# Kernel optimization log

Measured on AMD Instinct MI355X. Metric: run time of the kernel, lower is better.

The kernel has to match this reference:

```python
import jax, jax.numpy as jnp
import numpy as np

HEADS = 16

def split_heads(v, heads):
    # NOTE: faithful to the source: reshape [B,S,D] -> [B,S,h_dim,heads], then
    # transpose to [B,heads,S,h_dim]. This interleaves channels across heads
    # (different from the standard [B,S,heads,h_dim] split).
    B, S, D = v.shape
    hd = D // heads
    return v.reshape(B, S, hd, heads).transpose(0, 3, 1, 2)

def merge_heads(v):
    # [B,heads,S,h_dim] -> transpose [B,S,h_dim,heads] -> reshape [B,S,D]
    B, H, S, hd = v.shape
    return v.transpose(0, 2, 3, 1).reshape(B, S, H * hd)

def setup_inputs() -> dict:
    key = jax.random.key(0)
    ks = jax.random.split(key, 5)
    B, S, D = 2, 2048, 1024
    return {
        "x": jax.random.normal(ks[0], (B, S, D), dtype=jnp.float32),
        "qw": jax.random.normal(ks[1], (D, D), dtype=jnp.float32),
        "kw": jax.random.normal(ks[2], (D, D), dtype=jnp.float32),
        "vw": jax.random.normal(ks[3], (D, D), dtype=jnp.float32),
        "ow": jax.random.normal(ks[4], (D, D), dtype=jnp.float32),
    }

def reference(x, qw, kw, vw, ow):
    B, S, D = x.shape
    Q = split_heads(x @ qw, HEADS)  # [B,H,S,hd]
    K = split_heads(x @ kw, HEADS)
    V = split_heads(x @ vw, HEADS)
    # NOTE: scale is 1/sqrt(dim), NOT 1/sqrt(head_dim), as in the source.
    scale = 1.0 / jnp.sqrt(jnp.float32(D))
    score = jnp.einsum("bhqd,bhkd->bhqk", Q, K) * scale  # [B,H,S,S]
    causal = jnp.tril(jnp.ones((1, 1, S, S), dtype=score.dtype))
    score = score - 1e10 * (1.0 - causal)
    weights = jax.nn.softmax(score, axis=-1)
    attn = jnp.einsum("bhqk,bhkd->bhqd", weights, V)
    return merge_heads(attn) @ ow
```

## Files before the change

kernel.cpp:

```cpp
#include <hip/hip_runtime.h>


typedef __bf16 bf16x8 __attribute__((ext_vector_type(8)));
typedef float  f32x4  __attribute__((ext_vector_type(4)));

#define S_LEN  2048
#define DMODEL 1024
#define NHEADS 16
#define HDIM   64
#define LOG2E  1.44269504088896340736f

__device__ __forceinline__ void gll16(const __bf16* g, __bf16* l) {
    __builtin_amdgcn_global_load_lds(
        (const __attribute__((address_space(1))) unsigned int*)g,
        (__attribute__((address_space(3))) unsigned int*)l, 16, 0, 0);
}

__global__ __launch_bounds__(256) void conv_split(const float* __restrict__ x,
                                                  __bf16* __restrict__ hi,
                                                  __bf16* __restrict__ lo, int n4) {
    int i = blockIdx.x * 256 + threadIdx.x;
    if (i >= n4) return;
    float4 v = ((const float4*)x)[i];
    __bf16 h0 = (__bf16)v.x, h1 = (__bf16)v.y, h2 = (__bf16)v.z, h3 = (__bf16)v.w;
    bf16x8 dummy;
    (void)dummy;
    ushort4 hh, ll;
    hh.x = __builtin_bit_cast(unsigned short, h0);
    hh.y = __builtin_bit_cast(unsigned short, h1);
    hh.z = __builtin_bit_cast(unsigned short, h2);
    hh.w = __builtin_bit_cast(unsigned short, h3);
    ll.x = __builtin_bit_cast(unsigned short, (__bf16)(v.x - (float)h0));
    ll.y = __builtin_bit_cast(unsigned short, (__bf16)(v.y - (float)h1));
    ll.z = __builtin_bit_cast(unsigned short, (__bf16)(v.z - (float)h2));
    ll.w = __builtin_bit_cast(unsigned short, (__bf16)(v.w - (float)h3));
    ((ushort4*)hi)[i] = hh;
    ((ushort4*)lo)[i] = ll;
}

__global__ __launch_bounds__(256) void transpose_all(
    const float* __restrict__ qw, const float* __restrict__ kw,
    const float* __restrict__ vw, const float* __restrict__ ow,
    __bf16* __restrict__ qwthi, __bf16* __restrict__ qwtlo,
    __bf16* __restrict__ kwthi, __bf16* __restrict__ kwtlo,
    __bf16* __restrict__ vwt,  __bf16* __restrict__ owt) {
    __shared__ float tile[32][33];
    int z = blockIdx.z;
    const float* w = (z == 0) ? qw : (z == 1) ? kw : (z == 2) ? vw : ow;
    int n0 = blockIdx.x * 32, k0 = blockIdx.y * 32;
    int tx = threadIdx.x & 31, ty = threadIdx.x >> 5;
#pragma unroll
    for (int i = 0; i < 32; i += 8)
        tile[ty + i][tx] = w[(k0 + ty + i) * DMODEL + n0 + tx];
    __syncthreads();
#pragma unroll
    for (int i = 0; i < 32; i += 8) {
        float f = tile[tx][ty + i];
        int k = k0 + tx, n = n0 + ty + i;
        if (z <= 1) {
            __bf16 fh = (__bf16)f;
            __bf16 fl = (__bf16)(f - (float)fh);
            int c = (n & 15) * 64 + (n >> 4);
            if (z == 0) { qwthi[c * DMODEL + k] = fh; qwtlo[c * DMODEL + k] = fl; }
            else        { kwthi[c * DMODEL + k] = fh; kwtlo[c * DMODEL + k] = fl; }
        } else if (z == 2) {
            vwt[n * DMODEL + k] = (__bf16)f;
        } else {
            int ck = (k & 15) * 64 + (k >> 4);
            owt[n * DMODEL + ck] = (__bf16)f;
        }
    }
}

__global__ __launch_bounds__(256) void qkv_gemm(
    const __bf16* __restrict__ xhi, const __bf16* __restrict__ xlo,
    const __bf16* __restrict__ qwthi, const __bf16* __restrict__ qwtlo,
    const __bf16* __restrict__ kwthi, const __bf16* __restrict__ kwtlo,
    const __bf16* __restrict__ vwt,
    __bf16* __restrict__ Qhi, __bf16* __restrict__ Qlo,
    __bf16* __restrict__ Khi, __bf16* __restrict__ Klo,
    __bf16* __restrict__ Vt) {
    __shared__ __bf16 Ash[128][32], Asl[128][32], Bsh[128][32], Bsl[128][32];
    int mode = blockIdx.z;
    int tid  = threadIdx.x;
    int wave = tid >> 6, lane = tid & 63;
    int quad = lane >> 4, l15 = lane & 15;
    int wm = (wave >> 1) * 64, wn = (wave & 1) * 64;
    int grow = lane >> 2, gcol = (lane & 3) * 8;
    const int K = DMODEL;

    if (mode < 2) {
        const __bf16* Bh = mode ? kwthi : qwthi;
        const __bf16* Bl = mode ? kwtlo : qwtlo;
        int m0 = blockIdx.y * 128, n0 = blockIdx.x * 128;
        f32x4 acc[4][4] = {};
        for (int k0 = 0; k0 < K; k0 += 32) {
            __syncthreads();
#pragma unroll
            for (int ps = 0; ps < 2; ps++) {
                int row = ps * 64 + wave * 16;
                gll16(&xhi[(m0 + row + grow) * K + k0 + gcol], &Ash[row][0]);
                gll16(&xlo[(m0 + row + grow) * K + k0 + gcol], &Asl[row][0]);
                gll16(&Bh [(n0 + row + grow) * K + k0 + gcol], &Bsh[row][0]);
                gll16(&Bl [(n0 + row + grow) * K + k0 + gcol], &Bsl[row][0]);
            }
            __syncthreads();
            bf16x8 ah[4], al[4], bh[4], bl[4];
#pragma unroll
            for (int mi = 0; mi < 4; mi++) {
                ah[mi] = *(const bf16x8*)&Ash[wm + mi * 16 + l15][quad * 8];
                al[mi] = *(const bf16x8*)&Asl[wm + mi * 16 + l15][quad * 8];
            }
#pragma unroll
            for (int ni = 0; ni < 4; ni++) {
                bh[ni] = *(const bf16x8*)&Bsh[wn + ni * 16 + l15][quad * 8];
                bl[ni] = *(const bf16x8*)&Bsl[wn + ni * 16 + l15][quad * 8];
            }
#pragma unroll
            for (int mi = 0; mi < 4; mi++)
#pragma unroll
                for (int ni = 0; ni < 4; ni++) {
                    acc[mi][ni] = __builtin_amdgcn_mfma_f32_16x16x32_bf16(ah[mi], bh[ni], acc[mi][ni], 0, 0, 0);
                    acc[mi][ni] = __builtin_amdgcn_mfma_f32_16x16x32_bf16(ah[mi], bl[ni], acc[mi][ni], 0, 0, 0);
                    acc[mi][ni] = __builtin_amdgcn_mfma_f32_16x16x32_bf16(al[mi], bh[ni], acc[mi][ni], 0, 0, 0);
                }
        }
        float oscale = mode ? 1.0f : 0.03125f * LOG2E;
        __bf16* Ohi = mode ? Khi : Qhi;
        __bf16* Olo = mode ? Klo : Qlo;
#pragma unroll
        for (int mi = 0; mi < 4; mi++)
#pragma unroll
            for (int ni = 0; ni < 4; ni++)
#pragma unroll
                for (int rg = 0; rg < 4; rg++) {
                    int m = m0 + wm + mi * 16 + quad * 4 + rg;
                    int n = n0 + wn + ni * 16 + l15;
                    float v = acc[mi][ni][rg] * oscale;
                    size_t idx = (size_t)m * DMODEL + n;
                    __bf16 vh = (__bf16)v;
                    Ohi[idx] = vh;
                    Olo[idx] = (__bf16)(v - (float)vh);
                }
    } else {
        int ch0 = blockIdx.x * 128, xm0 = blockIdx.y * 128;
        f32x4 acc[4][4] = {};
        for (int k0 = 0; k0 < K; k0 += 32) {
            __syncthreads();
#pragma unroll
            for (int ps = 0; ps < 2; ps++) {
                int row = ps * 64 + wave * 16;
                gll16(&vwt[(ch0 + row + grow) * K + k0 + gcol], &Ash[row][0]);
                gll16(&xhi[(xm0 + row + grow) * K + k0 + gcol], &Bsh[row][0]);
            }
            __syncthreads();
            bf16x8 af[4], bfr[4];
#pragma unroll
            for (int mi = 0; mi < 4; mi++)
                af[mi] = *(const bf16x8*)&Ash[wm + mi * 16 + l15][quad * 8];
#pragma unroll
            for (int ni = 0; ni < 4; ni++)
                bfr[ni] = *(const bf16x8*)&Bsh[wn + ni * 16 + l15][quad * 8];
#pragma unroll
            for (int mi = 0; mi < 4; mi++)
#pragma unroll
                for (int ni = 0; ni < 4; ni++)
                    acc[mi][ni] = __builtin_amdgcn_mfma_f32_16x16x32_bf16(
                        af[mi], bfr[ni], acc[mi][ni], 0, 0, 0);
        }
#pragma unroll
        for (int mi = 0; mi < 4; mi++)
#pragma unroll
            for (int ni = 0; ni < 4; ni++)
#pragma unroll
                for (int rg = 0; rg < 4; rg++) {
                    int ch = ch0 + wm + mi * 16 + quad * 4 + rg;
                    int xm = xm0 + wn + ni * 16 + l15;
                    int b = xm >> 11, s = xm & 2047;
                    int h = ch & 15,  d = ch >> 4;
                    Vt[((size_t)(b * NHEADS + h) * HDIM + d) * S_LEN + s] =
                        (__bf16)acc[mi][ni][rg];
                }
    }
}

__global__ __launch_bounds__(256) void out_gemm(const __bf16* __restrict__ A,
                                                const __bf16* __restrict__ Bt,
                                                float* __restrict__ out) {
    __shared__ __bf16 As[64][32];
    __shared__ __bf16 Bs[128][32];
    int tid  = threadIdx.x;
    int wave = tid >> 6, lane = tid & 63;
    int quad = lane >> 4, l15 = lane & 15;
    int m0 = blockIdx.y * 64, n0 = blockIdx.x * 128;
    int wm = (wave >> 1) * 32, wn = (wave & 1) * 64;
    int grow = lane >> 2, gcol = (lane & 3) * 8;
    const int K = DMODEL;
    f32x4 acc[2][4] = {};

    for (int k0 = 0; k0 < K; k0 += 32) {
        __syncthreads();
        gll16(&A[(m0 + wave * 16 + grow) * K + k0 + gcol], &As[wave * 16][0]);
#pragma unroll
        for (int ps = 0; ps < 2; ps++) {
            int row = ps * 64 + wave * 16;
            gll16(&Bt[(n0 + row + grow) * K + k0 + gcol], &Bs[row][0]);
        }
        __syncthreads();
        bf16x8 af[2], bfr[4];
#pragma unroll
        for (int mi = 0; mi < 2; mi++)
            af[mi] = *(const bf16x8*)&As[wm + mi * 16 + l15][quad * 8];
#pragma unroll
        for (int ni = 0; ni < 4; ni++)
            bfr[ni] = *(const bf16x8*)&Bs[wn + ni * 16 + l15][quad * 8];
#pragma unroll
        for (int mi = 0; mi < 2; mi++)
#pragma unroll
            for (int ni = 0; ni < 4; ni++)
                acc[mi][ni] = __builtin_amdgcn_mfma_f32_16x16x32_bf16(
                    af[mi], bfr[ni], acc[mi][ni], 0, 0, 0);
    }

#pragma unroll
    for (int mi = 0; mi < 2; mi++)
#pragma unroll
        for (int ni = 0; ni < 4; ni++)
#pragma unroll
            for (int rg = 0; rg < 4; rg++) {
                int m = m0 + wm + mi * 16 + quad * 4 + rg;
                int n = n0 + wn + ni * 16 + l15;
                out[(size_t)m * DMODEL + n] = acc[mi][ni][rg];
            }
}

__global__ __launch_bounds__(256, 4) void flash_attn(const __bf16* __restrict__ Qhi,
                                                     const __bf16* __restrict__ Qlo,
                                                     const __bf16* __restrict__ Khi,
                                                     const __bf16* __restrict__ Klo,
                                                     const __bf16* __restrict__ Vt,
                                                     __bf16* __restrict__ attn) {
    int id  = blockIdx.x;
    int xcd = id & 7, r = id >> 3;
    int bh  = xcd + 8 * (r & 3);
    int t   = 31 - (r >> 2);
    int b = bh >> 4, h = bh & 15;
    const __bf16* Qh_hi = Qhi + (size_t)b * S_LEN * DMODEL + h * HDIM;
    const __bf16* Qh_lo = Qlo + (size_t)b * S_LEN * DMODEL + h * HDIM;
    const __bf16* Kh_hi = Khi + (size_t)b * S_LEN * DMODEL + h * HDIM;
    const __bf16* Kh_lo = Klo + (size_t)b * S_LEN * DMODEL + h * HDIM;
    const __bf16* Vh    = Vt  + (size_t)bh * HDIM * S_LEN;

    int tid = threadIdx.x, wave = tid >> 6, lane = tid & 63;
    int quad = lane >> 4, l15 = lane & 15;
    int iters = t + 1;

    __shared__ __bf16 KhF[8 * 64 * 8];
    __shared__ __bf16 KlF[8 * 64 * 8];
    __shared__ __bf16 VF [8 * 64 * 8];
    __shared__ __bf16 Ps[4][16][72];

    int c1  = tid >> 6, key = tid & 63;
    int inner = (c1 * 16 + (key & 15)) * 8;
    int rK    = (key >> 4);
    int kdst0 = rK * 512 + inner, kdst1 = (4 + rK) * 512 + inner;
    const __bf16* vrow = Vh + (size_t)key * S_LEN;

    int q0w = t * 64 + wave * 16;
    bf16x8 aqh0 = *(const bf16x8*)&Qh_hi[(size_t)(q0w + l15) * DMODEL + quad * 8];
    bf16x8 aqh1 = *(const bf16x8*)&Qh_hi[(size_t)(q0w + l15) * DMODEL + 32 + quad * 8];
    bf16x8 aql0 = *(const bf16x8*)&Qh_lo[(size_t)(q0w + l15) * DMODEL + quad * 8];
    bf16x8 aql1 = *(const bf16x8*)&Qh_lo[(size_t)(q0w + l15) * DMODEL + 32 + quad * 8];

    bf16x8 ones;
#pragma unroll
    for (int j = 0; j < 8; j++) ones[j] = (__bf16)1.0f;

    uint4 pk0, pk1, pl0, pl1, pv0, pv1;
    {
        const __bf16* sk = Kh_hi + (size_t)key * DMODEL;
        const __bf16* sl = Kh_lo + (size_t)key * DMODEL;
        pk0 = *(const uint4*)(sk + c1 * 8); pk1 = *(const uint4*)(sk + c1 * 8 + 32);
        pl0 = *(const uint4*)(sl + c1 * 8); pl1 = *(const uint4*)(sl + c1 * 8 + 32);
        pv0 = *(const uint4*)(vrow + c1 * 8); pv1 = *(const uint4*)(vrow + c1 * 8 + 32);
    }

    float m[4] = {-3e38f, -3e38f, -3e38f, -3e38f};
    f32x4 o[4] = {};
    f32x4 ol = {};
    int qrb = q0w + quad * 4;

    for (int i = 0; i < iters; i++) {
        int key0 = i * 64;
        bool diag = (i == iters - 1);

        __syncthreads();
        *(uint4*)&KhF[kdst0] = pk0;  *(uint4*)&KhF[kdst1] = pk1;
        *(uint4*)&KlF[kdst0] = pl0;  *(uint4*)&KlF[kdst1] = pl1;
        *(uint4*)&VF [kdst0] = pv0;  *(uint4*)&VF [kdst1] = pv1;
        __syncthreads();

        if (i + 1 < iters) {
            int key0n = (i + 1) * 64;
            const __bf16* sk = Kh_hi + (size_t)(key0n + key) * DMODEL;
            const __bf16* sl = Kh_lo + (size_t)(key0n + key) * DMODEL;
            pk0 = *(const uint4*)(sk + c1 * 8); pk1 = *(const uint4*)(sk + c1 * 8 + 32);
            pl0 = *(const uint4*)(sl + c1 * 8); pl1 = *(const uint4*)(sl + c1 * 8 + 32);
            pv0 = *(const uint4*)(vrow + key0n + c1 * 8);
            pv1 = *(const uint4*)(vrow + key0n + c1 * 8 + 32);
        }

        f32x4 sc[4] = {};
#pragma unroll
        for (int ni = 0; ni < 4; ni++) {
            bf16x8 kh0 = *(const bf16x8*)&KhF[(ni * 64 + lane) * 8];
            bf16x8 kh1 = *(const bf16x8*)&KhF[((4 + ni) * 64 + lane) * 8];
            bf16x8 kl0 = *(const bf16x8*)&KlF[(ni * 64 + lane) * 8];
            bf16x8 kl1 = *(const bf16x8*)&KlF[((4 + ni) * 64 + lane) * 8];
            sc[ni] = __builtin_amdgcn_mfma_f32_16x16x32_bf16(aqh0, kh0, sc[ni], 0, 0, 0);
            sc[ni] = __builtin_amdgcn_mfma_f32_16x16x32_bf16(aqh1, kh1, sc[ni], 0, 0, 0);
            sc[ni] = __builtin_amdgcn_mfma_f32_16x16x32_bf16(aqh0, kl0, sc[ni], 0, 0, 0);
            sc[ni] = __builtin_amdgcn_mfma_f32_16x16x32_bf16(aqh1, kl1, sc[ni], 0, 0, 0);
            sc[ni] = __builtin_amdgcn_mfma_f32_16x16x32_bf16(aql0, kh0, sc[ni], 0, 0, 0);
            sc[ni] = __builtin_amdgcn_mfma_f32_16x16x32_bf16(aql1, kh1, sc[ni], 0, 0, 0);
        }

        if (diag) {
#pragma unroll
            for (int ni = 0; ni < 4; ni++) {
                int keyi = key0 + ni * 16 + l15;
#pragma unroll
                for (int rg = 0; rg < 4; rg++)
                    if (keyi > qrb + rg) sc[ni][rg] = -1e30f;
            }
        }

#pragma unroll
        for (int rg = 0; rg < 4; rg++) {
            float mx = fmaxf(fmaxf(sc[0][rg], sc[1][rg]),
                             fmaxf(sc[2][rg], sc[3][rg]));
#pragma unroll
            for (int mm = 1; mm < 16; mm <<= 1)
                mx = fmaxf(mx, __shfl_xor(mx, mm, 64));
            float mnew  = fmaxf(m[rg], mx);
            float alpha = __builtin_amdgcn_exp2f(m[rg] - mnew);
            m[rg] = mnew;
#pragma unroll
            for (int ni = 0; ni < 4; ni++) {
                float px = __builtin_amdgcn_exp2f(sc[ni][rg] - mnew);
                Ps[wave][quad * 4 + rg][ni * 16 + l15] = (__bf16)px;
            }
            ol[rg] *= alpha;
#pragma unroll
            for (int ni = 0; ni < 4; ni++)
                o[ni][rg] *= alpha;
        }

#pragma unroll
        for (int step = 0; step < 2; step++) {
            bf16x8 ap = *(const bf16x8*)&Ps[wave][l15][step * 32 + quad * 8];
            ol = __builtin_amdgcn_mfma_f32_16x16x32_bf16(ap, ones, ol, 0, 0, 0);
#pragma unroll
            for (int ni = 0; ni < 4; ni++) {
                bf16x8 bv = *(const bf16x8*)&VF[((step * 4 + ni) * 64 + lane) * 8];
                o[ni] = __builtin_amdgcn_mfma_f32_16x16x32_bf16(ap, bv, o[ni], 0, 0, 0);
            }
        }
    }

#pragma unroll
    for (int rg = 0; rg < 4; rg++) {
        float inv = 1.0f / ol[rg];
        int q = q0w + quad * 4 + rg;
#pragma unroll
        for (int ni = 0; ni < 4; ni++) {
            attn[((size_t)b * S_LEN + q) * DMODEL + h * HDIM + ni * 16 + l15] =
                (__bf16)(o[ni][rg] * inv);
        }
    }
}

extern "C" void kernel_launch(void* const* d_in, const int* in_sizes, int n_in,
                              void* d_out, int out_size, void* d_ws, size_t ws_size,
                              hipStream_t stream) {
    const float* x  = (const float*)d_in[0];
    const float* qw = (const float*)d_in[1];
    const float* kw = (const float*)d_in[2];
    const float* vw = (const float*)d_in[3];
    const float* ow = (const float*)d_in[4];

    char* ws = (char*)d_ws;
    const size_t MB = 1024 * 1024;
    __bf16* xhi   = (__bf16*)(ws);
    __bf16* xlo   = (__bf16*)(ws + 8 * MB);
    __bf16* qwthi = (__bf16*)(ws + 16 * MB);
    __bf16* qwtlo = (__bf16*)(ws + 18 * MB);
    __bf16* kwthi = (__bf16*)(ws + 20 * MB);
    __bf16* kwtlo = (__bf16*)(ws + 22 * MB);
    __bf16* vwt   = (__bf16*)(ws + 24 * MB);
    __bf16* owt   = (__bf16*)(ws + 26 * MB);
    __bf16* Qhi_b = (__bf16*)(ws + 28 * MB);
    __bf16* Qlo_b = (__bf16*)(ws + 36 * MB);
    __bf16* Khi_b = (__bf16*)(ws + 44 * MB);
    __bf16* Klo_b = (__bf16*)(ws + 52 * MB);
    __bf16* Vtb   = (__bf16*)(ws + 60 * MB);
    __bf16* attnb = xlo;

    conv_split<<<4096, 256, 0, stream>>>(x, xhi, xlo, 4096 * 1024 / 4);
    transpose_all<<<dim3(32, 32, 4), 256, 0, stream>>>(
        qw, kw, vw, ow, qwthi, qwtlo, kwthi, kwtlo, vwt, owt);

    qkv_gemm<<<dim3(8, 32, 3), 256, 0, stream>>>(
        xhi, xlo, qwthi, qwtlo, kwthi, kwtlo, vwt,
        Qhi_b, Qlo_b, Khi_b, Klo_b, Vtb);

    flash_attn<<<1024, 256, 0, stream>>>(Qhi_b, Qlo_b, Khi_b, Klo_b, Vtb, attnb);

    out_gemm<<<dim3(8, 64), 256, 0, stream>>>(attnb, owt, (float*)d_out);
}
```

Baseline: 258.0 us.

## Double flash-attention query tile to 128 rows per block for K/V reuse

```diff
diff --git a/kernel.cpp b/kernel.cpp
--- a/kernel.cpp
+++ b/kernel.cpp
@@ -23,8 +23,6 @@
     if (i >= n4) return;
     float4 v = ((const float4*)x)[i];
     __bf16 h0 = (__bf16)v.x, h1 = (__bf16)v.y, h2 = (__bf16)v.z, h3 = (__bf16)v.w;
-    bf16x8 dummy;
-    (void)dummy;
     ushort4 hh, ll;
     hh.x = __builtin_bit_cast(unsigned short, h0);
     hh.y = __builtin_bit_cast(unsigned short, h1);
@@ -234,7 +232,7 @@
             }
 }
 
-__global__ __launch_bounds__(256, 4) void flash_attn(const __bf16* __restrict__ Qhi,
+__global__ __launch_bounds__(256, 3) void flash_attn(const __bf16* __restrict__ Qhi,
                                                      const __bf16* __restrict__ Qlo,
                                                      const __bf16* __restrict__ Khi,
                                                      const __bf16* __restrict__ Klo,
@@ -243,7 +241,7 @@
     int id  = blockIdx.x;
     int xcd = id & 7, r = id >> 3;
     int bh  = xcd + 8 * (r & 3);
-    int t   = 31 - (r >> 2);
+    int t   = 15 - (r >> 2);
     int b = bh >> 4, h = bh & 15;
     const __bf16* Qh_hi = Qhi + (size_t)b * S_LEN * DMODEL + h * HDIM;
     const __bf16* Qh_lo = Qlo + (size_t)b * S_LEN * DMODEL + h * HDIM;
@@ -253,12 +251,12 @@
 
     int tid = threadIdx.x, wave = tid >> 6, lane = tid & 63;
     int quad = lane >> 4, l15 = lane & 15;
-    int iters = t + 1;
+    int iters = 2 * t + 2;
 
     __shared__ __bf16 KhF[8 * 64 * 8];
     __shared__ __bf16 KlF[8 * 64 * 8];
     __shared__ __bf16 VF [8 * 64 * 8];
-    __shared__ __bf16 Ps[4][16][72];
+    __shared__ __bf16 Ps[4][32][72];
 
     int c1  = tid >> 6, key = tid & 63;
     int inner = (c1 * 16 + (key & 15)) * 8;
@@ -266,11 +264,16 @@
     int kdst0 = rK * 512 + inner, kdst1 = (4 + rK) * 512 + inner;
     const __bf16* vrow = Vh + (size_t)key * S_LEN;
 
-    int q0w = t * 64 + wave * 16;
-    bf16x8 aqh0 = *(const bf16x8*)&Qh_hi[(size_t)(q0w + l15) * DMODEL + quad * 8];
-    bf16x8 aqh1 = *(const bf16x8*)&Qh_hi[(size_t)(q0w + l15) * DMODEL + 32 + quad * 8];
-    bf16x8 aql0 = *(const bf16x8*)&Qh_lo[(size_t)(q0w + l15) * DMODEL + quad * 8];
-    bf16x8 aql1 = *(const bf16x8*)&Qh_lo[(size_t)(q0w + l15) * DMODEL + 32 + quad * 8];
+    int q0w = t * 128 + wave * 32;
+    bf16x8 aqh0[2], aqh1[2], aql0[2], aql1[2];
+#pragma unroll
+    for (int mi = 0; mi < 2; mi++) {
+        size_t qr = (size_t)(q0w + mi * 16 + l15) * DMODEL;
+        aqh0[mi] = *(const bf16x8*)&Qh_hi[qr + quad * 8];
+        aqh1[mi] = *(const bf16x8*)&Qh_hi[qr + 32 + quad * 8];
+        aql0[mi] = *(const bf16x8*)&Qh_lo[qr + quad * 8];
+        aql1[mi] = *(const bf16x8*)&Qh_lo[qr + 32 + quad * 8];
+    }
 
     bf16x8 ones;
 #pragma unroll
@@ -285,14 +288,13 @@
         pv0 = *(const uint4*)(vrow + c1 * 8); pv1 = *(const uint4*)(vrow + c1 * 8 + 32);
     }
 
-    float m[4] = {-3e38f, -3e38f, -3e38f, -3e38f};
-    f32x4 o[4] = {};
-    f32x4 ol = {};
-    int qrb = q0w + quad * 4;
+    float m[2][4] = {{-3e38f, -3e38f, -3e38f, -3e38f},
+                     {-3e38f, -3e38f, -3e38f, -3e38f}};
+    f32x4 o[2][4] = {};
+    f32x4 ol[2] = {};
 
     for (int i = 0; i < iters; i++) {
         int key0 = i * 64;
-        bool diag = (i == iters - 1);
 
         __syncthreads();
         *(uint4*)&KhF[kdst0] = pk0;  *(uint4*)&KhF[kdst1] = pk1;
@@ -310,74 +312,85 @@
             pv1 = *(const uint4*)(vrow + key0n + c1 * 8 + 32);
         }
 
-        f32x4 sc[4] = {};
+        f32x4 sc[2][4] = {};
 #pragma unroll
         for (int ni = 0; ni < 4; ni++) {
             bf16x8 kh0 = *(const bf16x8*)&KhF[(ni * 64 + lane) * 8];
             bf16x8 kh1 = *(const bf16x8*)&KhF[((4 + ni) * 64 + lane) * 8];
             bf16x8 kl0 = *(const bf16x8*)&KlF[(ni * 64 + lane) * 8];
             bf16x8 kl1 = *(const bf16x8*)&KlF[((4 + ni) * 64 + lane) * 8];
-            sc[ni] = __builtin_amdgcn_mfma_f32_16x16x32_bf16(aqh0, kh0, sc[ni], 0, 0, 0);
-            sc[ni] = __builtin_amdgcn_mfma_f32_16x16x32_bf16(aqh1, kh1, sc[ni], 0, 0, 0);
-            sc[ni] = __builtin_amdgcn_mfma_f32_16x16x32_bf16(aqh0, kl0, sc[ni], 0, 0, 0);
-            sc[ni] = __builtin_amdgcn_mfma_f32_16x16x32_bf16(aqh1, kl1, sc[ni], 0, 0, 0);
-            sc[ni] = __builtin_amdgcn_mfma_f32_16x16x32_bf16(aql0, kh0, sc[ni], 0, 0, 0);
-            sc[ni] = __builtin_amdgcn_mfma_f32_16x16x32_bf16(aql1, kh1, sc[ni], 0, 0, 0);
-        }
-
-        if (diag) {
-#pragma unroll
-            for (int ni = 0; ni < 4; ni++) {
-                int keyi = key0 + ni * 16 + l15;
-#pragma unroll
-                for (int rg = 0; rg < 4; rg++)
-                    if (keyi > qrb + rg) sc[ni][rg] = -1e30f;
-            }
-        }
-
-#pragma unroll
-        for (int rg = 0; rg < 4; rg++) {
-            float mx = fmaxf(fmaxf(sc[0][rg], sc[1][rg]),
-                             fmaxf(sc[2][rg], sc[3][rg]));
-#pragma unroll
-            for (int mm = 1; mm < 16; mm <<= 1)
-                mx = fmaxf(mx, __shfl_xor(mx, mm, 64));
-            float mnew  = fmaxf(m[rg], mx);
-            float alpha = __builtin_amdgcn_exp2f(m[rg] - mnew);
-            m[rg] = mnew;
-#pragma unroll
-            for (int ni = 0; ni < 4; ni++) {
-                float px = __builtin_amdgcn_exp2f(sc[ni][rg] - mnew);
-                Ps[wave][quad * 4 + rg][ni * 16 + l15] = (__bf16)px;
-            }
-            ol[rg] *= alpha;
-#pragma unroll
-            for (int ni = 0; ni < 4; ni++)
-                o[ni][rg] *= alpha;
+#pragma unroll
+            for (int mi = 0; mi < 2; mi++) {
+                sc[mi][ni] = __builtin_amdgcn_mfma_f32_16x16x32_bf16(aqh0[mi], kh0, sc[mi][ni], 0, 0, 0);
+                sc[mi][ni] = __builtin_amdgcn_mfma_f32_16x16x32_bf16(aqh1[mi], kh1, sc[mi][ni], 0, 0, 0);
+                sc[mi][ni] = __builtin_amdgcn_mfma_f32_16x16x32_bf16(aqh0[mi], kl0, sc[mi][ni], 0, 0, 0);
+                sc[mi][ni] = __builtin_amdgcn_mfma_f32_16x16x32_bf16(aqh1[mi], kl1, sc[mi][ni], 0, 0, 0);
+                sc[mi][ni] = __builtin_amdgcn_mfma_f32_16x16x32_bf16(aql0[mi], kh0, sc[mi][ni], 0, 0, 0);
+                sc[mi][ni] = __builtin_amdgcn_mfma_f32_16x16x32_bf16(aql1[mi], kh1, sc[mi][ni], 0, 0, 0);
+            }
+        }
+
+#pragma unroll
+        for (int mi = 0; mi < 2; mi++) {
+            int qrb = q0w + mi * 16 + quad * 4;
+            if (key0 + 63 > qrb) {
+#pragma unroll
+                for (int ni = 0; ni < 4; ni++) {
+                    int keyi = key0 + ni * 16 + l15;
+#pragma unroll
+                    for (int rg = 0; rg < 4; rg++)
+                        if (keyi > qrb + rg) sc[mi][ni][rg] = -1e30f;
+                }
+            }
+#pragma unroll
+            for (int rg = 0; rg < 4; rg++) {
+                float mx = fmaxf(fmaxf(sc[mi][0][rg], sc[mi][1][rg]),
+                                 fmaxf(sc[mi][2][rg], sc[mi][3][rg]));
+#pragma unroll
+                for (int mm = 1; mm < 16; mm <<= 1)
+                    mx = fmaxf(mx, __shfl_xor(mx, mm, 64));
+                float mnew  = fmaxf(m[mi][rg], mx);
+                float alpha = __builtin_amdgcn_exp2f(m[mi][rg] - mnew);
+                m[mi][rg] = mnew;
+#pragma unroll
+                for (int ni = 0; ni < 4; ni++) {
+                    float px = __builtin_amdgcn_exp2f(sc[mi][ni][rg] - mnew);
+                    Ps[wave][mi * 16 + quad * 4 + rg][ni * 16 + l15] = (__bf16)px;
+                }
+                ol[mi][rg] *= alpha;
+#pragma unroll
+                for (int ni = 0; ni < 4; ni++)
+                    o[mi][ni][rg] *= alpha;
+            }
         }
 
 #pragma unroll
         for (int step = 0; step < 2; step++) {
-            bf16x8 ap = *(const bf16x8*)&Ps[wave][l15][step * 32 + quad * 8];
-            ol = __builtin_amdgcn_mfma_f32_16x16x32_bf16(ap, ones, ol, 0, 0, 0);
+            bf16x8 ap0 = *(const bf16x8*)&Ps[wave][l15][step * 32 + quad * 8];
+            bf16x8 ap1 = *(const bf16x8*)&Ps[wave][16 + l15][step * 32 + quad * 8];
+            ol[0] = __builtin_amdgcn_mfma_f32_16x16x32_bf16(ap0, ones, ol[0], 0, 0, 0);
+            ol[1] = __builtin_amdgcn_mfma_f32_16x16x32_bf16(ap1, ones, ol[1], 0, 0, 0);
 #pragma unroll
             for (int ni = 0; ni < 4; ni++) {
                 bf16x8 bv = *(const bf16x8*)&VF[((step * 4 + ni) * 64 + lane) * 8];
-                o[ni] = __builtin_amdgcn_mfma_f32_16x16x32_bf16(ap, bv, o[ni], 0, 0, 0);
-            }
-        }
-    }
-
-#pragma unroll
-    for (int rg = 0; rg < 4; rg++) {
-        float inv = 1.0f / ol[rg];
-        int q = q0w + quad * 4 + rg;
-#pragma unroll
-        for (int ni = 0; ni < 4; ni++) {
-            attn[((size_t)b * S_LEN + q) * DMODEL + h * HDIM + ni * 16 + l15] =
-                (__bf16)(o[ni][rg] * inv);
-        }
-    }
+                o[0][ni] = __builtin_amdgcn_mfma_f32_16x16x32_bf16(ap0, bv, o[0][ni], 0, 0, 0);
+                o[1][ni] = __builtin_amdgcn_mfma_f32_16x16x32_bf16(ap1, bv, o[1][ni], 0, 0, 0);
+            }
+        }
+    }
+
+#pragma unroll
+    for (int mi = 0; mi < 2; mi++)
+#pragma unroll
+        for (int rg = 0; rg < 4; rg++) {
+            float inv = 1.0f / ol[mi][rg];
+            int q = q0w + mi * 16 + quad * 4 + rg;
+#pragma unroll
+            for (int ni = 0; ni < 4; ni++) {
+                attn[((size_t)b * S_LEN + q) * DMODEL + h * HDIM + ni * 16 + l15] =
+                    (__bf16)(o[mi][ni][rg] * inv);
+            }
+        }
 }
 
 extern "C" void kernel_launch(void* const* d_in, const int* in_sizes, int n_in,
@@ -414,7 +427,7 @@
         xhi, xlo, qwthi, qwtlo, kwthi, kwtlo, vwt,
         Qhi_b, Qlo_b, Khi_b, Klo_b, Vtb);
 
-    flash_attn<<<1024, 256, 0, stream>>>(Qhi_b, Qlo_b, Khi_b, Klo_b, Vtb, attnb);
+    flash_attn<<<512, 256, 0, stream>>>(Qhi_b, Qlo_b, Khi_b, Klo_b, Vtb, attnb);
 
     out_gemm<<<dim3(8, 64), 256, 0, stream>>>(attnb, owt, (float*)d_out);
 }
```

After: 325.8 us. 26.3% more time.

## Merge prep kernels into one launch and fuse Q/K projections sharing x tiles

Applied to the files above, without the earlier changes.

```diff
diff --git a/kernel.cpp b/kernel.cpp
--- a/kernel.cpp
+++ b/kernel.cpp
@@ -16,38 +16,38 @@
         (__attribute__((address_space(3))) unsigned int*)l, 16, 0, 0);
 }
 
-__global__ __launch_bounds__(256) void conv_split(const float* __restrict__ x,
-                                                  __bf16* __restrict__ hi,
-                                                  __bf16* __restrict__ lo, int n4) {
-    int i = blockIdx.x * 256 + threadIdx.x;
-    if (i >= n4) return;
-    float4 v = ((const float4*)x)[i];
-    __bf16 h0 = (__bf16)v.x, h1 = (__bf16)v.y, h2 = (__bf16)v.z, h3 = (__bf16)v.w;
-    bf16x8 dummy;
-    (void)dummy;
-    ushort4 hh, ll;
-    hh.x = __builtin_bit_cast(unsigned short, h0);
-    hh.y = __builtin_bit_cast(unsigned short, h1);
-    hh.z = __builtin_bit_cast(unsigned short, h2);
-    hh.w = __builtin_bit_cast(unsigned short, h3);
-    ll.x = __builtin_bit_cast(unsigned short, (__bf16)(v.x - (float)h0));
-    ll.y = __builtin_bit_cast(unsigned short, (__bf16)(v.y - (float)h1));
-    ll.z = __builtin_bit_cast(unsigned short, (__bf16)(v.z - (float)h2));
-    ll.w = __builtin_bit_cast(unsigned short, (__bf16)(v.w - (float)h3));
-    ((ushort4*)hi)[i] = hh;
-    ((ushort4*)lo)[i] = ll;
-}
-
-__global__ __launch_bounds__(256) void transpose_all(
+__global__ __launch_bounds__(256) void prep_all(
+    const float* __restrict__ x,
     const float* __restrict__ qw, const float* __restrict__ kw,
     const float* __restrict__ vw, const float* __restrict__ ow,
+    __bf16* __restrict__ xhi, __bf16* __restrict__ xlo,
     __bf16* __restrict__ qwthi, __bf16* __restrict__ qwtlo,
     __bf16* __restrict__ kwthi, __bf16* __restrict__ kwtlo,
     __bf16* __restrict__ vwt,  __bf16* __restrict__ owt) {
     __shared__ float tile[32][33];
-    int z = blockIdx.z;
+    int id = blockIdx.x;
+    if (id < 4096) {
+        int i = id * 256 + threadIdx.x;
+        float4 v = ((const float4*)x)[i];
+        __bf16 h0 = (__bf16)v.x, h1 = (__bf16)v.y, h2 = (__bf16)v.z, h3 = (__bf16)v.w;
+        ushort4 hh, ll;
+        hh.x = __builtin_bit_cast(unsigned short, h0);
+        hh.y = __builtin_bit_cast(unsigned short, h1);
+        hh.z = __builtin_bit_cast(unsigned short, h2);
+        hh.w = __builtin_bit_cast(unsigned short, h3);
+        ll.x = __builtin_bit_cast(unsigned short, (__bf16)(v.x - (float)h0));
+        ll.y = __builtin_bit_cast(unsigned short, (__bf16)(v.y - (float)h1));
+        ll.z = __builtin_bit_cast(unsigned short, (__bf16)(v.z - (float)h2));
+        ll.w = __builtin_bit_cast(unsigned short, (__bf16)(v.w - (float)h3));
+        ((ushort4*)xhi)[i] = hh;
+        ((ushort4*)xlo)[i] = ll;
+        return;
+    }
+    int rid = id - 4096;
+    int z = rid >> 10;
+    int bx = rid & 31, by = (rid >> 5) & 31;
     const float* w = (z == 0) ? qw : (z == 1) ? kw : (z == 2) ? vw : ow;
-    int n0 = blockIdx.x * 32, k0 = blockIdx.y * 32;
+    int n0 = bx * 32, k0 = by * 32;
     int tx = threadIdx.x & 31, ty = threadIdx.x >> 5;
 #pragma unroll
     for (int i = 0; i < 32; i += 8)
@@ -80,8 +80,8 @@
     __bf16* __restrict__ Qhi, __bf16* __restrict__ Qlo,
     __bf16* __restrict__ Khi, __bf16* __restrict__ Klo,
     __bf16* __restrict__ Vt) {
-    __shared__ __bf16 Ash[128][32], Asl[128][32], Bsh[128][32], Bsl[128][32];
-    int mode = blockIdx.z;
+    __shared__ __bf16 Ash[128][32], Asl[128][32];
+    __shared__ __bf16 Bqh[128][32], Bql[128][32], Bkh[128][32], Bkl[128][32];
     int tid  = threadIdx.x;
     int wave = tid >> 6, lane = tid & 63;
     int quad = lane >> 4, l15 = lane & 15;
@@ -89,23 +89,23 @@
     int grow = lane >> 2, gcol = (lane & 3) * 8;
     const int K = DMODEL;
 
-    if (mode < 2) {
-        const __bf16* Bh = mode ? kwthi : qwthi;
-        const __bf16* Bl = mode ? kwtlo : qwtlo;
+    if (blockIdx.z == 0) {
         int m0 = blockIdx.y * 128, n0 = blockIdx.x * 128;
-        f32x4 acc[4][4] = {};
+        f32x4 accQ[4][4] = {}, accK[4][4] = {};
         for (int k0 = 0; k0 < K; k0 += 32) {
             __syncthreads();
 #pragma unroll
             for (int ps = 0; ps < 2; ps++) {
                 int row = ps * 64 + wave * 16;
-                gll16(&xhi[(m0 + row + grow) * K + k0 + gcol], &Ash[row][0]);
-                gll16(&xlo[(m0 + row + grow) * K + k0 + gcol], &Asl[row][0]);
-                gll16(&Bh [(n0 + row + grow) * K + k0 + gcol], &Bsh[row][0]);
-                gll16(&Bl [(n0 + row + grow) * K + k0 + gcol], &Bsl[row][0]);
+                gll16(&xhi  [(m0 + row + grow) * K + k0 + gcol], &Ash[row][0]);
+                gll16(&xlo  [(m0 + row + grow) * K + k0 + gcol], &Asl[row][0]);
+                gll16(&qwthi[(n0 + row + grow) * K + k0 + gcol], &Bqh[row][0]);
+                gll16(&qwtlo[(n0 + row + grow) * K + k0 + gcol], &Bql[row][0]);
+                gll16(&kwthi[(n0 + row + grow) * K + k0 + gcol], &Bkh[row][0]);
+                gll16(&kwtlo[(n0 + row + grow) * K + k0 + gcol], &Bkl[row][0]);
             }
             __syncthreads();
-            bf16x8 ah[4], al[4], bh[4], bl[4];
+            bf16x8 ah[4], al[4];
 #pragma unroll
             for (int mi = 0; mi < 4; mi++) {
                 ah[mi] = *(const bf16x8*)&Ash[wm + mi * 16 + l15][quad * 8];
@@ -113,21 +113,25 @@
             }
 #pragma unroll
             for (int ni = 0; ni < 4; ni++) {
-                bh[ni] = *(const bf16x8*)&Bsh[wn + ni * 16 + l15][quad * 8];
-                bl[ni] = *(const bf16x8*)&Bsl[wn + ni * 16 + l15][quad * 8];
-            }
-#pragma unroll
-            for (int mi = 0; mi < 4; mi++)
-#pragma unroll
-                for (int ni = 0; ni < 4; ni++) {
-                    acc[mi][ni] = __builtin_amdgcn_mfma_f32_16x16x32_bf16(ah[mi], bh[ni], acc[mi][ni], 0, 0, 0);
-                    acc[mi][ni] = __builtin_amdgcn_mfma_f32_16x16x32_bf16(ah[mi], bl[ni], acc[mi][ni], 0, 0, 0);
-                    acc[mi][ni] = __builtin_amdgcn_mfma_f32_16x16x32_bf16(al[mi], bh[ni], acc[mi][ni], 0, 0, 0);
+                bf16x8 bh = *(const bf16x8*)&Bqh[wn + ni * 16 + l15][quad * 8];
+                bf16x8 bl = *(const bf16x8*)&Bql[wn + ni * 16 + l15][quad * 8];
+#pragma unroll
+                for (int mi = 0; mi < 4; mi++) {
+                    accQ[mi][ni] = __builtin_amdgcn_mfma_f32_16x16x32_bf16(ah[mi], bh, accQ[mi][ni], 0, 0, 0);
+                    accQ[mi][ni] = __builtin_amdgcn_mfma_f32_16x16x32_bf16(ah[mi], bl, accQ[mi][ni], 0, 0, 0);
+                    accQ[mi][ni] = __builtin_amdgcn_mfma_f32_16x16x32_bf16(al[mi], bh, accQ[mi][ni], 0, 0, 0);
                 }
-        }
-        float oscale = mode ? 1.0f : 0.03125f * LOG2E;
-        __bf16* Ohi = mode ? Khi : Qhi;
-        __bf16* Olo = mode ? Klo : Qlo;
+                bh = *(const bf16x8*)&Bkh[wn + ni * 16 + l15][quad * 8];
+                bl = *(const bf16x8*)&Bkl[wn + ni * 16 + l15][quad * 8];
+#pragma unroll
+                for (int mi = 0; mi < 4; mi++) {
+                    accK[mi][ni] = __builtin_amdgcn_mfma_f32_16x16x32_bf16(ah[mi], bh, accK[mi][ni], 0, 0, 0);
+                    accK[mi][ni] = __builtin_amdgcn_mfma_f32_16x16x32_bf16(ah[mi], bl, accK[mi][ni], 0, 0, 0);
+                    accK[mi][ni] = __builtin_amdgcn_mfma_f32_16x16x32_bf16(al[mi], bh, accK[mi][ni], 0, 0, 0);
+                }
+            }
+        }
+        const float qscale = 0.03125f * LOG2E;
 #pragma unroll
         for (int mi = 0; mi < 4; mi++)
 #pragma unroll
@@ -136,11 +140,15 @@
                 for (int rg = 0; rg < 4; rg++) {
                     int m = m0 + wm + mi * 16 + quad * 4 + rg;
                     int n = n0 + wn + ni * 16 + l15;
-                    float v = acc[mi][ni][rg] * oscale;
                     size_t idx = (size_t)m * DMODEL + n;
-                    __bf16 vh = (__bf16)v;
-                    Ohi[idx] = vh;
-                    Olo[idx] = (__bf16)(v - (float)vh);
+                    float vq = accQ[mi][ni][rg] * qscale;
+                    __bf16 vqh = (__bf16)vq;
+                    Qhi[idx] = vqh;
+                    Qlo[idx] = (__bf16)(vq - (float)vqh);
+                    float vk = accK[mi][ni][rg];
+                    __bf16 vkh = (__bf16)vk;
+                    Khi[idx] = vkh;
+                    Klo[idx] = (__bf16)(vk - (float)vkh);
                 }
     } else {
         int ch0 = blockIdx.x * 128, xm0 = blockIdx.y * 128;
@@ -151,7 +159,7 @@
             for (int ps = 0; ps < 2; ps++) {
                 int row = ps * 64 + wave * 16;
                 gll16(&vwt[(ch0 + row + grow) * K + k0 + gcol], &Ash[row][0]);
-                gll16(&xhi[(xm0 + row + grow) * K + k0 + gcol], &Bsh[row][0]);
+                gll16(&xhi[(xm0 + row + grow) * K + k0 + gcol], &Bqh[row][0]);
             }
             __syncthreads();
             bf16x8 af[4], bfr[4];
@@ -160,7 +168,7 @@
                 af[mi] = *(const bf16x8*)&Ash[wm + mi * 16 + l15][quad * 8];
 #pragma unroll
             for (int ni = 0; ni < 4; ni++)
-                bfr[ni] = *(const bf16x8*)&Bsh[wn + ni * 16 + l15][quad * 8];
+                bfr[ni] = *(const bf16x8*)&Bqh[wn + ni * 16 + l15][quad * 8];
 #pragma unroll
             for (int mi = 0; mi < 4; mi++)
 #pragma unroll
@@ -406,11 +414,11 @@
     __bf16* Vtb   = (__bf16*)(ws + 60 * MB);
     __bf16* attnb = xlo;
 
-    conv_split<<<4096, 256, 0, stream>>>(x, xhi, xlo, 4096 * 1024 / 4);
-    transpose_all<<<dim3(32, 32, 4), 256, 0, stream>>>(
-        qw, kw, vw, ow, qwthi, qwtlo, kwthi, kwtlo, vwt, owt);
-
-    qkv_gemm<<<dim3(8, 32, 3), 256, 0, stream>>>(
+    prep_all<<<8192, 256, 0, stream>>>(x, qw, kw, vw, ow,
+                                       xhi, xlo, qwthi, qwtlo, kwthi, kwtlo,
+                                       vwt, owt);
+
+    qkv_gemm<<<dim3(8, 32, 2), 256, 0, stream>>>(
         xhi, xlo, qwthi, qwtlo, kwthi, kwtlo, vwt,
         Qhi_b, Qlo_b, Khi_b, Klo_b, Vtb);
 
```

After: 275.3 us. 6.7% more time.

## Merge prep kernels into one launch and swizzle GEMM LDS tiles

Applied to the files above, without the earlier changes.

```diff
diff --git a/kernel.cpp b/kernel.cpp
--- a/kernel.cpp
+++ b/kernel.cpp
@@ -16,38 +16,38 @@
         (__attribute__((address_space(3))) unsigned int*)l, 16, 0, 0);
 }
 
-__global__ __launch_bounds__(256) void conv_split(const float* __restrict__ x,
-                                                  __bf16* __restrict__ hi,
-                                                  __bf16* __restrict__ lo, int n4) {
-    int i = blockIdx.x * 256 + threadIdx.x;
-    if (i >= n4) return;
-    float4 v = ((const float4*)x)[i];
-    __bf16 h0 = (__bf16)v.x, h1 = (__bf16)v.y, h2 = (__bf16)v.z, h3 = (__bf16)v.w;
-    bf16x8 dummy;
-    (void)dummy;
-    ushort4 hh, ll;
-    hh.x = __builtin_bit_cast(unsigned short, h0);
-    hh.y = __builtin_bit_cast(unsigned short, h1);
-    hh.z = __builtin_bit_cast(unsigned short, h2);
-    hh.w = __builtin_bit_cast(unsigned short, h3);
-    ll.x = __builtin_bit_cast(unsigned short, (__bf16)(v.x - (float)h0));
-    ll.y = __builtin_bit_cast(unsigned short, (__bf16)(v.y - (float)h1));
-    ll.z = __builtin_bit_cast(unsigned short, (__bf16)(v.z - (float)h2));
-    ll.w = __builtin_bit_cast(unsigned short, (__bf16)(v.w - (float)h3));
-    ((ushort4*)hi)[i] = hh;
-    ((ushort4*)lo)[i] = ll;
-}
-
-__global__ __launch_bounds__(256) void transpose_all(
+__global__ __launch_bounds__(256) void prep_all(
+    const float* __restrict__ x,
     const float* __restrict__ qw, const float* __restrict__ kw,
     const float* __restrict__ vw, const float* __restrict__ ow,
+    __bf16* __restrict__ xhi, __bf16* __restrict__ xlo,
     __bf16* __restrict__ qwthi, __bf16* __restrict__ qwtlo,
     __bf16* __restrict__ kwthi, __bf16* __restrict__ kwtlo,
     __bf16* __restrict__ vwt,  __bf16* __restrict__ owt) {
     __shared__ float tile[32][33];
-    int z = blockIdx.z;
+    int id = blockIdx.x;
+    if (id < 4096) {
+        int i = id * 256 + threadIdx.x;
+        float4 v = ((const float4*)x)[i];
+        __bf16 h0 = (__bf16)v.x, h1 = (__bf16)v.y, h2 = (__bf16)v.z, h3 = (__bf16)v.w;
+        ushort4 hh, ll;
+        hh.x = __builtin_bit_cast(unsigned short, h0);
+        hh.y = __builtin_bit_cast(unsigned short, h1);
+        hh.z = __builtin_bit_cast(unsigned short, h2);
+        hh.w = __builtin_bit_cast(unsigned short, h3);
+        ll.x = __builtin_bit_cast(unsigned short, (__bf16)(v.x - (float)h0));
+        ll.y = __builtin_bit_cast(unsigned short, (__bf16)(v.y - (float)h1));
+        ll.z = __builtin_bit_cast(unsigned short, (__bf16)(v.z - (float)h2));
+        ll.w = __builtin_bit_cast(unsigned short, (__bf16)(v.w - (float)h3));
+        ((ushort4*)xhi)[i] = hh;
+        ((ushort4*)xlo)[i] = ll;
+        return;
+    }
+    int rid = id - 4096;
+    int z = rid >> 10;
+    int bx = rid & 31, by = (rid >> 5) & 31;
     const float* w = (z == 0) ? qw : (z == 1) ? kw : (z == 2) ? vw : ow;
-    int n0 = blockIdx.x * 32, k0 = blockIdx.y * 32;
+    int n0 = bx * 32, k0 = by * 32;
     int tx = threadIdx.x & 31, ty = threadIdx.x >> 5;
 #pragma unroll
     for (int i = 0; i < 32; i += 8)
@@ -86,7 +86,9 @@
     int wave = tid >> 6, lane = tid & 63;
     int quad = lane >> 4, l15 = lane & 15;
     int wm = (wave >> 1) * 64, wn = (wave & 1) * 64;
-    int grow = lane >> 2, gcol = (lane & 3) * 8;
+    int grow = lane >> 2;
+    int gcol = (((lane & 3) - ((lane >> 3) & 3)) & 3) * 8;
+    int sA   = ((quad + (l15 >> 1)) & 3) * 8;
     const int K = DMODEL;
 
     if (mode < 2) {
@@ -108,13 +110,13 @@
             bf16x8 ah[4], al[4], bh[4], bl[4];
 #pragma unroll
             for (int mi = 0; mi < 4; mi++) {
-                ah[mi] = *(const bf16x8*)&Ash[wm + mi * 16 + l15][quad * 8];
-                al[mi] = *(const bf16x8*)&Asl[wm + mi * 16 + l15][quad * 8];
+                ah[mi] = *(const bf16x8*)&Ash[wm + mi * 16 + l15][sA];
+                al[mi] = *(const bf16x8*)&Asl[wm + mi * 16 + l15][sA];
             }
 #pragma unroll
             for (int ni = 0; ni < 4; ni++) {
-                bh[ni] = *(const bf16x8*)&Bsh[wn + ni * 16 + l15][quad * 8];
-                bl[ni] = *(const bf16x8*)&Bsl[wn + ni * 16 + l15][quad * 8];
+                bh[ni] = *(const bf16x8*)&Bsh[wn + ni * 16 + l15][sA];
+                bl[ni] = *(const bf16x8*)&Bsl[wn + ni * 16 + l15][sA];
             }
 #pragma unroll
             for (int mi = 0; mi < 4; mi++)
@@ -157,10 +159,10 @@
             bf16x8 af[4], bfr[4];
 #pragma unroll
             for (int mi = 0; mi < 4; mi++)
-                af[mi] = *(const bf16x8*)&Ash[wm + mi * 16 + l15][quad * 8];
+                af[mi] = *(const bf16x8*)&Ash[wm + mi * 16 + l15][sA];
 #pragma unroll
             for (int ni = 0; ni < 4; ni++)
-                bfr[ni] = *(const bf16x8*)&Bsh[wn + ni * 16 + l15][quad * 8];
+                bfr[ni] = *(const bf16x8*)&Bsh[wn + ni * 16 + l15][sA];
 #pragma unroll
             for (int mi = 0; mi < 4; mi++)
 #pragma unroll
@@ -194,7 +196,9 @@
     int quad = lane >> 4, l15 = lane & 15;
     int m0 = blockIdx.y * 64, n0 = blockIdx.x * 128;
     int wm = (wave >> 1) * 32, wn = (wave & 1) * 64;
-    int grow = lane >> 2, gcol = (lane & 3) * 8;
+    int grow = lane >> 2;
+    int gcol = (((lane & 3) - ((lane >> 3) & 3)) & 3) * 8;
+    int sA   = ((quad + (l15 >> 1)) & 3) * 8;
     const int K = DMODEL;
     f32x4 acc[2][4] = {};
 
@@ -210,10 +214,10 @@
         bf16x8 af[2], bfr[4];
 #pragma unroll
         for (int mi = 0; mi < 2; mi++)
-            af[mi] = *(const bf16x8*)&As[wm + mi * 16 + l15][quad * 8];
+            af[mi] = *(const bf16x8*)&As[wm + mi * 16 + l15][sA];
 #pragma unroll
         for (int ni = 0; ni < 4; ni++)
-            bfr[ni] = *(const bf16x8*)&Bs[wn + ni * 16 + l15][quad * 8];
+            bfr[ni] = *(const bf16x8*)&Bs[wn + ni * 16 + l15][sA];
 #pragma unroll
         for (int mi = 0; mi < 2; mi++)
 #pragma unroll
@@ -406,9 +410,9 @@
     __bf16* Vtb   = (__bf16*)(ws + 60 * MB);
     __bf16* attnb = xlo;
 
-    conv_split<<<4096, 256, 0, stream>>>(x, xhi, xlo, 4096 * 1024 / 4);
-    transpose_all<<<dim3(32, 32, 4), 256, 0, stream>>>(
-        qw, kw, vw, ow, qwthi, qwtlo, kwthi, kwtlo, vwt, owt);
+    prep_all<<<8192, 256, 0, stream>>>(x, qw, kw, vw, ow,
+                                       xhi, xlo, qwthi, qwtlo, kwthi, kwtlo,
+                                       vwt, owt);
 
     qkv_gemm<<<dim3(8, 32, 3), 256, 0, stream>>>(
         xhi, xlo, qwthi, qwtlo, kwthi, kwtlo, vwt,
```

New measurement: 248.0 us. 3.9% less time.
